# Performance work log

Measured on AMD Instinct MI355X. Metric: run time of the kernel, lower is better.

Reference implementation:

```python
import jax, jax.numpy as jnp
import numpy as np

N, E, G = 50000, 800000, 512
IN_DIM, EDGE_DIM, HID, OUT_DIM, HEADS = 16, 8, 32, 64, 4
NEG_SLOPE = 0.2


def _glorot(key, shape):
    fan_in, fan_out = shape[0], shape[-1]
    lim = jnp.sqrt(6.0 / (fan_in + fan_out))
    return jax.random.uniform(key, shape, jnp.float32, -lim, lim)


def setup_inputs() -> dict:
    key = jax.random.key(0)
    ks = jax.random.split(key, 32)
    inp = {
        "x": jax.random.normal(ks[0], (N, IN_DIM), jnp.float32),
        "edge_src": jax.random.randint(ks[1], (E,), 0, N, jnp.int32),
        "edge_dst": jax.random.randint(ks[2], (E,), 0, N, jnp.int32),
        "edge_attr": jax.random.normal(ks[3], (E, EDGE_DIM), jnp.float32),
        "batch": jnp.sort(jax.random.randint(ks[4], (N,), 0, G, jnp.int32)),
    }
    # layer 1: in=16 -> heads=4, C=32
    inp["W1s"] = _glorot(ks[5], (IN_DIM, HEADS * HID)); inp["W1d"] = _glorot(ks[6], (IN_DIM, HEADS * HID))
    inp["W1e"] = _glorot(ks[7], (EDGE_DIM, HEADS * HID))
    inp["b1s"] = jnp.zeros((HEADS * HID,)); inp["b1d"] = jnp.zeros((HEADS * HID,))
    inp["att1"] = _glorot(ks[8], (HEADS, HID)); inp["bias1"] = jnp.zeros((HEADS * HID,))
    # layer 2: in=128 -> heads=4, C=32
    D2 = HEADS * HID
    inp["W2s"] = _glorot(ks[9], (D2, HEADS * HID)); inp["W2d"] = _glorot(ks[10], (D2, HEADS * HID))
    inp["W2e"] = _glorot(ks[11], (EDGE_DIM, HEADS * HID))
    inp["b2s"] = jnp.zeros((HEADS * HID,)); inp["b2d"] = jnp.zeros((HEADS * HID,))
    inp["att2"] = _glorot(ks[12], (HEADS, HID)); inp["bias2"] = jnp.zeros((HEADS * HID,))
    # layer 3: in=128 -> heads=1, C=32
    inp["W3s"] = _glorot(ks[13], (D2, HID)); inp["W3d"] = _glorot(ks[14], (D2, HID))
    inp["W3e"] = _glorot(ks[15], (EDGE_DIM, HID))
    inp["b3s"] = jnp.zeros((HID,)); inp["b3d"] = jnp.zeros((HID,))
    inp["att3"] = _glorot(ks[16], (1, HID)); inp["bias3"] = jnp.zeros((HID,))
    # MLP: 32 -> 64 -> 64
    inp["Wm1"] = _glorot(ks[17], (HID, 2 * HID)); inp["bm1"] = jnp.zeros((2 * HID,))
    inp["Wm2"] = _glorot(ks[18], (2 * HID, OUT_DIM)); inp["bm2"] = jnp.zeros((OUT_DIM,))
    return inp


def gatv2_conv(x, src, dst, edge_attr, Ws, Wd, We, bs, bd, att, bias, heads, ch):
    n = x.shape[0]
    xs = (x @ Ws + bs).reshape(n, heads, ch)   # lin_l (source / value)
    xd = (x @ Wd + bd).reshape(n, heads, ch)   # lin_r (target)
    ea = (edge_attr @ We).reshape(-1, heads, ch)
    z = jax.nn.leaky_relu(xs[src] + xd[dst] + ea, NEG_SLOPE)       # [E,H,C]
    e = jnp.einsum('ehc,hc->eh', z, att)                           # [E,H]
    m = jax.ops.segment_max(e, dst, num_segments=n)                # scatter-softmax over dst
    p = jnp.exp(e - m[dst])
    denom = jax.ops.segment_sum(p, dst, num_segments=n)
    alpha = p / denom[dst]                                          # [E,H]
    msg = xs[src] * alpha[:, :, None]                               # [E,H,C]
    out = jax.ops.segment_sum(msg, dst, num_segments=n)
    return out.reshape(n, heads * ch) + bias


def reference(x, edge_src, edge_dst, edge_attr, batch,
              W1s, W1d, W1e, b1s, b1d, att1, bias1,
              W2s, W2d, W2e, b2s, b2d, att2, bias2,
              W3s, W3d, W3e, b3s, b3d, att3, bias3,
              Wm1, bm1, Wm2, bm2):
    h = jax.nn.elu(gatv2_conv(x, edge_src, edge_dst, edge_attr, W1s, W1d, W1e, b1s, b1d, att1, bias1, HEADS, HID))
    h = jax.nn.elu(gatv2_conv(h, edge_src, edge_dst, edge_attr, W2s, W2d, W2e, b2s, b2d, att2, bias2, HEADS, HID))
    h = gatv2_conv(h, edge_src, edge_dst, edge_attr, W3s, W3d, W3e, b3s, b3d, att3, bias3, 1, HID)
    # global mean pool over graphs
    sums = jax.ops.segment_sum(h, batch, num_segments=G)
    cnt = jax.ops.segment_sum(jnp.ones((h.shape[0],), h.dtype), batch, num_segments=G)
    emb = sums / jnp.maximum(cnt, 1.0)[:, None]
    return jax.nn.relu(emb @ Wm1 + bm1) @ Wm2 + bm2
```

## Files before the change

### kernel.cpp

```cpp
#include <hip/hip_runtime.h>
#include <cstdint>
#include <cstddef>

constexpr int kN = 50000;
constexpr int kE = 800000;
constexpr int kG = 512;
constexpr float kNegSlope = 0.2f;
constexpr float kLog2e = 1.4426950408889634f;

typedef float f4v __attribute__((ext_vector_type(4)));
typedef _Float16 h2v __attribute__((ext_vector_type(2)));
typedef _Float16 h4v __attribute__((ext_vector_type(4)));
typedef _Float16 h8v __attribute__((ext_vector_type(8)));

#if defined(__has_builtin)
#if __has_builtin(__builtin_amdgcn_fdot2)
#define HAS_FDOT2 1
#endif
#if __has_builtin(__builtin_amdgcn_exp2f)
#define HAS_EXP2 1
#endif
#endif

__device__ inline float dot2f(h2v a, h2v b, float c) {
#ifdef HAS_FDOT2
  return __builtin_amdgcn_fdot2(a, b, c, false);
#else
  return c + (float)a.x * (float)b.x + (float)a.y * (float)b.y;
#endif
}

#ifdef HAS_EXP2
#define ATT_SC kLog2e
__device__ inline float fexp(float x) { return __builtin_amdgcn_exp2f(x); }
#else
#define ATT_SC 1.0f
__device__ inline float fexp(float x) { return __expf(x); }
#endif


constexpr int kRec = 32;

__global__ void k_hist(const int* __restrict__ dst, int* __restrict__ counts,
                       int* __restrict__ pos, int n) {
  int i = blockIdx.x * blockDim.x + threadIdx.x;
  if (i < n) pos[i] = atomicAdd(&counts[dst[i]], 1);
}

__global__ __launch_bounds__(256) void k_scan_blk(const int* __restrict__ counts,
                                                  int* __restrict__ excl,
                                                  int* __restrict__ bsums, int n) {
  __shared__ int sh[256];
  int tid = threadIdx.x;
  int i = blockIdx.x * 256 + tid;
  int c = (i < n) ? counts[i] : 0;
  sh[tid] = c;
  __syncthreads();
  for (int off = 1; off < 256; off <<= 1) {
    int t = (tid >= off) ? sh[tid - off] : 0;
    __syncthreads();
    sh[tid] += t;
    __syncthreads();
  }
  if (i < n) excl[i] = sh[tid] - c;
  if (tid == 255) bsums[blockIdx.x] = sh[255];
}

__global__ __launch_bounds__(256) void k_scan_add(const int* __restrict__ excl,
                                                  const int* __restrict__ bsums,
                                                  int* __restrict__ row_ptr,
                                                  int n, int nb) {
  __shared__ int sh[256];
  int tid = threadIdx.x;
  int c = (tid < nb) ? bsums[tid] : 0;
  sh[tid] = c;
  __syncthreads();
  for (int off = 1; off < 256; off <<= 1) {
    int t = (tid >= off) ? sh[tid - off] : 0;
    __syncthreads();
    sh[tid] += t;
    __syncthreads();
  }
  int top = (blockIdx.x > 0) ? sh[blockIdx.x - 1] : 0;
  int total = sh[nb - 1];
  __syncthreads();
  int i = blockIdx.x * 256 + tid;
  if (i < n) row_ptr[i] = excl[i] + top;
  if (i == n) row_ptr[n] = total;
}

__global__ void k_scatter(const int* __restrict__ src, const int* __restrict__ dst,
                          const float* __restrict__ eattr,
                          const int* __restrict__ row_ptr, const int* __restrict__ pos,
                          char* __restrict__ csr, int n) {
  int i = blockIdx.x * blockDim.x + threadIdx.x;
  if (i >= n) return;
  int p = row_ptr[dst[i]] + pos[i];
  const float4* s4 = (const float4*)eattr + (size_t)i * 2;
  float4 a = s4[0];
  float4 b = s4[1];
  h8v hv;
  hv[0] = (_Float16)a.x; hv[1] = (_Float16)a.y; hv[2] = (_Float16)a.z; hv[3] = (_Float16)a.w;
  hv[4] = (_Float16)b.x; hv[5] = (_Float16)b.y; hv[6] = (_Float16)b.z; hv[7] = (_Float16)b.w;
  char* r = csr + (size_t)p * kRec;
  *(h8v*)r = hv;
  *(uint32_t*)(r + 16) = (uint32_t)src[i];
}

__global__ __launch_bounds__(256) void k_prep(
    const float* __restrict__ x,
    const float* __restrict__ W1s, const float* __restrict__ W1d,
    const float* __restrict__ W2s, const float* __restrict__ W2d,
    const float* __restrict__ W3s, const float* __restrict__ W3d,
    const float* __restrict__ W1e, const float* __restrict__ W2e,
    const float* __restrict__ W3e,
    const int* __restrict__ batch, int* __restrict__ gptr,
    int* __restrict__ counts,
    _Float16* __restrict__ xf, _Float16* __restrict__ Wt1,
    _Float16* __restrict__ Wt2, _Float16* __restrict__ Wt3,
    _Float16* __restrict__ We1t, _Float16* __restrict__ We2t,
    _Float16* __restrict__ We3t, int n) {
  int i = blockIdx.x * 256 + threadIdx.x;
  if (i < n) {
    counts[i] = 0;
    int b1 = batch[i];
    int b0 = (i == 0) ? -1 : batch[i - 1];
    for (int g = b0 + 1; g <= b1; ++g) gptr[g] = i;
    if (i == n - 1) {
      for (int g = b1 + 1; g <= kG; ++g) gptr[g] = n;
    }
  }
  i -= n;
  if (i < 0) return;
  int r0 = n * 4;
  if (i < r0) {
    int node = i >> 2, j = i & 3;
    h8v v;
    if (j < 2) {
      const float4* xp = (const float4*)(x + node * 16 + j * 8);
      float4 a = xp[0], b = xp[1];
      v[0] = (_Float16)a.x; v[1] = (_Float16)a.y; v[2] = (_Float16)a.z; v[3] = (_Float16)a.w;
      v[4] = (_Float16)b.x; v[5] = (_Float16)b.y; v[6] = (_Float16)b.z; v[7] = (_Float16)b.w;
    } else {
#pragma unroll
      for (int q = 0; q < 8; ++q) v[q] = (_Float16)0.f;
    }
    *(h8v*)(xf + (size_t)node * 32 + j * 8) = v;
    return;
  }
  i -= r0;
  if (i < 256 * 32) {
    int c = i >> 5, k = i & 31;
    const float* W = (c < 128) ? W1s : W1d;
    Wt1[i] = (k < 16) ? (_Float16)W[k * 128 + (c & 127)] : (_Float16)0.f;
    return;
  }
  i -= 256 * 32;
  if (i < 256 * 128) {
    int c = i >> 7, k = i & 127;
    const float* W = (c < 128) ? W2s : W2d;
    Wt2[i] = (_Float16)W[k * 128 + (c & 127)];
    return;
  }
  i -= 256 * 128;
  if (i < 64 * 128) {
    int c = i >> 7, k = i & 127;
    const float* W = (c < 32) ? W3s : W3d;
    int cc = (c < 32) ? c : c - 32;
    Wt3[i] = (_Float16)W[k * 32 + cc];
    return;
  }
  i -= 64 * 128;
  if (i < 128 * 8) {
    We1t[i] = (_Float16)W1e[(i & 7) * 128 + (i >> 3)];
    return;
  }
  i -= 128 * 8;
  if (i < 128 * 8) {
    We2t[i] = (_Float16)W2e[(i & 7) * 128 + (i >> 3)];
    return;
  }
  i -= 128 * 8;
  if (i < 32 * 8) {
    We3t[i] = (_Float16)W3e[(i & 7) * 32 + (i >> 3)];
  }
}

template <int KT, int NC2>
__global__ __launch_bounds__(256) void k_tmfma(
    const _Float16* __restrict__ hf, const _Float16* __restrict__ Wt,
    const float* __restrict__ bs, const float* __restrict__ bd,
    _Float16* __restrict__ xs_h, _Float16* __restrict__ xd_h, int n_nodes) {
  constexpr int K = KT * 32;
  constexpr int NCS = NC2 / 2;
  constexpr int D = NCS * 16;
  int lane = threadIdx.x & 63;
  int wid = threadIdx.x >> 6;
  int m = lane & 15;
  int quad = lane >> 4;
  int base = (blockIdx.x * 4 + wid) * 16;
  if (base >= n_nodes) return;
  int arow = min(base + m, n_nodes - 1);

  h8v a[KT];
#pragma unroll
  for (int t = 0; t < KT; ++t)
    a[t] = *(const h8v*)(hf + (size_t)arow * K + t * 32 + quad * 8);

  bool full = (base + 16 <= n_nodes);
#pragma unroll
  for (int c = 0; c < NC2; ++c) {
    f4v acc = {0.f, 0.f, 0.f, 0.f};
#pragma unroll
    for (int t = 0; t < KT; ++t) {
      h8v b = *(const h8v*)(Wt + (size_t)(c * 16 + m) * K + t * 32 + quad * 8);
      acc = __builtin_amdgcn_mfma_f32_16x16x32_f16(a[t], b, acc, 0, 0, 0);
    }
    float bv = (c < NCS) ? bs[c * 16 + m] : bd[(c - NCS) * 16 + m];
#pragma unroll
    for (int r = 0; r < 4; ++r) {
      int node = base + quad * 4 + r;
      if (full || node < n_nodes) {
        if (c < NCS)
          xs_h[(size_t)node * D + c * 16 + m] = (_Float16)(acc[r] + bv);
        else
          xd_h[(size_t)node * D + (c - NCS) * 16 + m] = (_Float16)(acc[r] + bv);
      }
    }
  }
}

template <bool DO_ELU>
__global__ __launch_bounds__(64) void k_gat128(
    const int* __restrict__ row_ptr, const char* __restrict__ csr,
    const _Float16* __restrict__ xs_h, const _Float16* __restrict__ xd_h,
    const float* __restrict__ att, const float* __restrict__ bias,
    const _Float16* __restrict__ Wet, _Float16* __restrict__ hout, int n_nodes) {
  __shared__ _Float16 sea[64 * 8];
  int lane = threadIdx.x & 63;
  int node = blockIdx.x;
  if (node >= n_nodes) return;
  int slot = lane >> 5;
  int sl = lane & 31;
  int ch0 = sl * 4;

  float4 at4 = *(const float4*)(att + ch0);
  float atl[4] = {at4.x * ATT_SC, at4.y * ATT_SC, at4.z * ATT_SC, at4.w * ATT_SC};
  h2v we[4][4];
#pragma unroll
  for (int c = 0; c < 4; ++c) {
    h8v wv = *(const h8v*)(Wet + (size_t)(ch0 + c) * 8);
#pragma unroll
    for (int t = 0; t < 4; ++t) {
      h2v w;
      w[0] = wv[2 * t];
      w[1] = wv[2 * t + 1];
      we[c][t] = w;
    }
  }
  float4 bv4 = *(const float4*)(bias + ch0);
  float bl[4] = {bv4.x, bv4.y, bv4.z, bv4.w};

  h4v xdh = *(const h4v*)(xd_h + (size_t)node * 128 + ch0);
  float xdl[4];
#pragma unroll
  for (int c = 0; c < 4; ++c) xdl[c] = (float)xdh[c];

  const char* xsb = (const char*)xs_h;
  uint32_t chb = (uint32_t)sl * 8u;

  float acc[4] = {0.f, 0.f, 0.f, 0.f};
  float l_run = 0.f;
  int beg = row_ptr[node], end = row_ptr[node + 1];

  for (int cbeg = beg; cbeg < end; cbeg += 64) {
    int cnt = min(end - cbeg, 64);
    int sv = 0;
    if (lane < cnt) {
      const char* r = csr + (size_t)(cbeg + lane) * kRec;
      h8v t = __builtin_nontemporal_load((const h8v*)r);
      sv = (int)__builtin_nontemporal_load((const uint32_t*)(r + 16));
      *(h8v*)&sea[lane * 8] = t;
    }

    auto addr = [&](int i) -> uint32_t {
      int s = __shfl(sv, i + slot, 64);
      return (uint32_t)s * 256u + chb;
    };
    auto consume = [&](int i, h4v xh) {
      int e = i + slot;
      const h2v* pe = (const h2v*)&sea[e * 8];
      h2v a0 = pe[0], a1 = pe[1], a2 = pe[2], a3 = pe[3];
      float xf[4];
#pragma unroll
      for (int c = 0; c < 4; ++c) xf[c] = (float)xh[c];
      float sc = 0.f;
#pragma unroll
      for (int c = 0; c < 4; ++c) {
        float z = dot2f(a3, we[c][3],
                  dot2f(a2, we[c][2],
                  dot2f(a1, we[c][1],
                  dot2f(a0, we[c][0], xf[c] + xdl[c]))));
        z = fmaxf(z, kNegSlope * z);
        sc = fmaf(z, atl[c], sc);
      }
      sc += __shfl_xor(sc, 1, 64);
      sc += __shfl_xor(sc, 2, 64);
      sc += __shfl_xor(sc, 4, 64);
      float p = (e < cnt) ? fexp(sc) : 0.f;
      l_run += p;
#pragma unroll
      for (int c = 0; c < 4; ++c) acc[c] += p * xf[c];
    };

    uint32_t oa = addr(0), ob = addr(2);
    h4v xa = *(const h4v*)(xsb + oa);
    h4v xb = *(const h4v*)(xsb + ob);
    for (int i = 0; i < cnt; i += 4) {
      bool pf = (i + 4 < cnt);
      h4v pa, pb;
      if (pf) {
        uint32_t na = addr(i + 4), nb = addr(i + 6);
        pa = *(const h4v*)(xsb + na);
        pb = *(const h4v*)(xsb + nb);
      }
      consume(i, xa);
      consume(i + 2, xb);
      if (pf) { xa = pa; xb = pb; }
    }
  }

  l_run += __shfl_xor(l_run, 32, 64);
#pragma unroll
  for (int c = 0; c < 4; ++c) acc[c] += __shfl_xor(acc[c], 32, 64);

  if (slot == 0) {
    float inv = (l_run > 0.f) ? (1.f / l_run) : 0.f;
    h4v ov;
#pragma unroll
    for (int c = 0; c < 4; ++c) {
      float o = acc[c] * inv + bl[c];
      if (DO_ELU) o = (o > 0.f) ? o : (__expf(o) - 1.f);
      ov[c] = (_Float16)o;
    }
    __builtin_nontemporal_store(ov, (h4v*)(hout + (size_t)node * 128 + ch0));
  }
}

template <bool DO_ELU>
__global__ __launch_bounds__(64) void k_gat32(
    const int* __restrict__ row_ptr, const char* __restrict__ csr,
    const _Float16* __restrict__ xs_h, const _Float16* __restrict__ xd_h,
    const float* __restrict__ att, const float* __restrict__ bias,
    const _Float16* __restrict__ Wet, _Float16* __restrict__ hout, int n_nodes) {
  __shared__ _Float16 sea[32 * 8];
  int lane = threadIdx.x & 63;
  int node = blockIdx.x;
  if (node >= n_nodes) return;
  int slot = lane >> 3;
  int sl = lane & 7;
  int ch0 = sl * 4;

  float4 at4 = *(const float4*)(att + ch0);
  float atl[4] = {at4.x * ATT_SC, at4.y * ATT_SC, at4.z * ATT_SC, at4.w * ATT_SC};
  h2v we[4][4];
#pragma unroll
  for (int c = 0; c < 4; ++c) {
    h8v wv = *(const h8v*)(Wet + (size_t)(ch0 + c) * 8);
#pragma unroll
    for (int t = 0; t < 4; ++t) {
      h2v w;
      w[0] = wv[2 * t];
      w[1] = wv[2 * t + 1];
      we[c][t] = w;
    }
  }
  float4 bv4 = *(const float4*)(bias + ch0);
  float bl[4] = {bv4.x, bv4.y, bv4.z, bv4.w};

  h4v xdh = *(const h4v*)(xd_h + (size_t)node * 32 + ch0);
  float xdl[4];
#pragma unroll
  for (int c = 0; c < 4; ++c) xdl[c] = (float)xdh[c];

  const char* xsb = (const char*)xs_h;
  uint32_t chb = (uint32_t)sl * 8u;

  float acc[4] = {0.f, 0.f, 0.f, 0.f};
  float l_run = 0.f;
  int beg = row_ptr[node], end = row_ptr[node + 1];

  for (int cbeg = beg; cbeg < end; cbeg += 32) {
    int cnt = min(end - cbeg, 32);
    int sv = 0;
    if (lane < cnt) {
      const char* r = csr + (size_t)(cbeg + lane) * kRec;
      h8v t = __builtin_nontemporal_load((const h8v*)r);
      sv = (int)__builtin_nontemporal_load((const uint32_t*)(r + 16));
      *(h8v*)&sea[lane * 8] = t;
    }

    auto addr = [&](int i) -> uint32_t {
      int idx = (i + slot) & 31;
      int s = __shfl(sv, idx, 64);
      return (uint32_t)s * 64u + chb;
    };
    auto consume = [&](int i, h4v xh) {
      int e = i + slot;
      const h2v* pe = (const h2v*)&sea[e * 8];
      h2v a0 = pe[0], a1 = pe[1], a2 = pe[2], a3 = pe[3];
      float xf[4];
#pragma unroll
      for (int c = 0; c < 4; ++c) xf[c] = (float)xh[c];
      float sc = 0.f;
#pragma unroll
      for (int c = 0; c < 4; ++c) {
        float z = dot2f(a3, we[c][3],
                  dot2f(a2, we[c][2],
                  dot2f(a1, we[c][1],
                  dot2f(a0, we[c][0], xf[c] + xdl[c]))));
        z = fmaxf(z, kNegSlope * z);
        sc = fmaf(z, atl[c], sc);
      }
      sc += __shfl_xor(sc, 1, 64);
      sc += __shfl_xor(sc, 2, 64);
      sc += __shfl_xor(sc, 4, 64);
      float p = (e < cnt) ? fexp(sc) : 0.f;
      l_run += p;
#pragma unroll
      for (int c = 0; c < 4; ++c) acc[c] += p * xf[c];
    };

    uint32_t oa = addr(0), ob = addr(8);
    h4v xa = *(const h4v*)(xsb + oa);
    h4v xb = *(const h4v*)(xsb + ob);
    for (int i = 0; i < cnt; i += 16) {
      bool pf = (i + 16 < cnt);
      h4v pa, pb;
      if (pf) {
        uint32_t na = addr(i + 16), nb = addr(i + 24);
        pa = *(const h4v*)(xsb + na);
        pb = *(const h4v*)(xsb + nb);
      }
      consume(i, xa);
      consume(i + 8, xb);
      if (pf) { xa = pa; xb = pb; }
    }
  }

#pragma unroll
  for (int off = 8; off < 64; off <<= 1) {
    l_run += __shfl_xor(l_run, off, 64);
#pragma unroll
    for (int c = 0; c < 4; ++c) acc[c] += __shfl_xor(acc[c], off, 64);
  }

  if (slot == 0) {
    float inv = (l_run > 0.f) ? (1.f / l_run) : 0.f;
    h4v ov;
#pragma unroll
    for (int c = 0; c < 4; ++c) {
      float o = acc[c] * inv + bl[c];
      if (DO_ELU) o = (o > 0.f) ? o : (__expf(o) - 1.f);
      ov[c] = (_Float16)o;
    }
    __builtin_nontemporal_store(ov, (h4v*)(hout + (size_t)node * 32 + ch0));
  }
}

__global__ __launch_bounds__(64) void k_pool_mlp(
    const _Float16* __restrict__ h3, const int* __restrict__ gptr,
    const float* __restrict__ Wm1, const float* __restrict__ bm1,
    const float* __restrict__ Wm2, const float* __restrict__ bm2,
    float* __restrict__ out, int n_nodes) {
  int g = blockIdx.x;
  int t = threadIdx.x;
  int lo = gptr[g];
  int hi = gptr[g + 1];
  int c = t & 31, half = t >> 5;
  float sum = 0.f;
  for (int i = lo + half; i < hi; i += 2) sum += (float)h3[(size_t)i * 32 + c];
  sum += __shfl_xor(sum, 32, 64);
  float cnt = (float)(hi - lo);
  float emb = sum / fmaxf(cnt, 1.f);
  __shared__ float sh_emb[32];
  __shared__ float sh_hid[64];
  if (half == 0) sh_emb[c] = emb;
  __syncthreads();
  float hv = bm1[t];
  for (int k = 0; k < 32; ++k) hv += sh_emb[k] * Wm1[k * 64 + t];
  hv = fmaxf(hv, 0.f);
  sh_hid[t] = hv;
  __syncthreads();
  float ov = bm2[t];
  for (int k = 0; k < 64; ++k) ov += sh_hid[k] * Wm2[k * 64 + t];
  out[(size_t)g * 64 + t] = ov;
}

extern "C" void kernel_launch(void* const* d_in, const int* in_sizes, int n_in,
                              void* d_out, int out_size, void* d_ws, size_t ws_size,
                              hipStream_t stream) {
  const float* x = (const float*)d_in[0];
  const int* esrc = (const int*)d_in[1];
  const int* edst = (const int*)d_in[2];
  const float* eattr = (const float*)d_in[3];
  const int* batch = (const int*)d_in[4];
  const float* W1s = (const float*)d_in[5];
  const float* W1d = (const float*)d_in[6];
  const float* W1e = (const float*)d_in[7];
  const float* b1s = (const float*)d_in[8];
  const float* b1d = (const float*)d_in[9];
  const float* att1 = (const float*)d_in[10];
  const float* bias1 = (const float*)d_in[11];
  const float* W2s = (const float*)d_in[12];
  const float* W2d = (const float*)d_in[13];
  const float* W2e = (const float*)d_in[14];
  const float* b2s = (const float*)d_in[15];
  const float* b2d = (const float*)d_in[16];
  const float* att2 = (const float*)d_in[17];
  const float* bias2 = (const float*)d_in[18];
  const float* W3s = (const float*)d_in[19];
  const float* W3d = (const float*)d_in[20];
  const float* W3e = (const float*)d_in[21];
  const float* b3s = (const float*)d_in[22];
  const float* b3d = (const float*)d_in[23];
  const float* att3 = (const float*)d_in[24];
  const float* bias3 = (const float*)d_in[25];
  const float* Wm1 = (const float*)d_in[26];
  const float* bm1 = (const float*)d_in[27];
  const float* Wm2 = (const float*)d_in[28];
  const float* bm2 = (const float*)d_in[29];

  constexpr int kNB = (kN + 255) / 256;

  char* p = (char*)d_ws;
  auto take = [&](size_t bytes) {
    char* r = p;
    p += (bytes + 255) & ~(size_t)255;
    return r;
  };
  int* row_ptr = (int*)take((size_t)(kN + 1) * sizeof(int));
  int* counts = (int*)take((size_t)kN * sizeof(int));
  int* pos = (int*)take((size_t)kE * sizeof(int));
  int* excl = (int*)take((size_t)kN * sizeof(int));
  int* bsums = (int*)take((size_t)kNB * sizeof(int));
  int* gptr = (int*)take((size_t)(kG + 1) * sizeof(int));
  char* csr = take((size_t)kE * kRec);
  _Float16* xf = (_Float16*)take((size_t)kN * 32 * sizeof(_Float16));
  _Float16* Wt1 = (_Float16*)take((size_t)256 * 32 * sizeof(_Float16));
  _Float16* Wt2 = (_Float16*)take((size_t)256 * 128 * sizeof(_Float16));
  _Float16* Wt3 = (_Float16*)take((size_t)64 * 128 * sizeof(_Float16));
  _Float16* We1t = (_Float16*)take((size_t)128 * 8 * sizeof(_Float16));
  _Float16* We2t = (_Float16*)take((size_t)128 * 8 * sizeof(_Float16));
  _Float16* We3t = (_Float16*)take((size_t)32 * 8 * sizeof(_Float16));
  _Float16* xs_h = (_Float16*)take((size_t)kN * 128 * sizeof(_Float16));
  _Float16* xd_h = (_Float16*)take((size_t)kN * 128 * sizeof(_Float16));
  _Float16* hA = (_Float16*)take((size_t)kN * 128 * sizeof(_Float16));
  _Float16* hB = (_Float16*)take((size_t)kN * 128 * sizeof(_Float16));
  _Float16* h3 = (_Float16*)take((size_t)kN * 32 * sizeof(_Float16));

  {
    int prep_total = kN + kN * 4 + 256 * 32 + 256 * 128 + 64 * 128 +
                     128 * 8 + 128 * 8 + 32 * 8;
    k_prep<<<(prep_total + 255) / 256, 256, 0, stream>>>(
        x, W1s, W1d, W2s, W2d, W3s, W3d, W1e, W2e, W3e,
        batch, gptr, counts, xf, Wt1, Wt2, Wt3, We1t, We2t, We3t, kN);
  }
  k_hist<<<(kE + 255) / 256, 256, 0, stream>>>(edst, counts, pos, kE);
  k_scan_blk<<<kNB, 256, 0, stream>>>(counts, excl, bsums, kN);
  k_scan_add<<<(kN + 1 + 255) / 256, 256, 0, stream>>>(excl, bsums, row_ptr, kN, kNB);
  k_scatter<<<(kE + 255) / 256, 256, 0, stream>>>(esrc, edst, eattr, row_ptr, pos,
                                                  csr, kE);

  constexpr int kTB = (kN + 63) / 64;

  k_tmfma<1, 16><<<kTB, 256, 0, stream>>>(xf, Wt1, b1s, b1d, xs_h, xd_h, kN);
  k_gat128<true><<<kN, 64, 0, stream>>>(row_ptr, csr, xs_h, xd_h,
                                        att1, bias1, We1t, hA, kN);
  k_tmfma<4, 16><<<kTB, 256, 0, stream>>>(hA, Wt2, b2s, b2d, xs_h, xd_h, kN);
  k_gat128<true><<<kN, 64, 0, stream>>>(row_ptr, csr, xs_h, xd_h,
                                        att2, bias2, We2t, hB, kN);
  k_tmfma<4, 4><<<kTB, 256, 0, stream>>>(hB, Wt3, b3s, b3d, xs_h, xd_h, kN);
  k_gat32<false><<<kN, 64, 0, stream>>>(row_ptr, csr, xs_h, xd_h,
                                        att3, bias3, We3t, h3, kN);
  k_pool_mlp<<<kG, 64, 0, stream>>>(h3, gptr, Wm1, bm1, Wm2, bm2, (float*)d_out, kN);
}
```

Before: 411.0 us.

## Drop nontemporal hints, write full CSR record tail, widen pooling kernel

Three unrelated tweaks. The CSR record tail is now written as one 16-byte store with zero padding instead of a lone 4-byte store, so each record fill is a full-line write. The GAT kernels switch their nontemporal loads and stores to ordinary ones, so CSR records and hidden activations that are reused across the three layers can stay in cache. The pool+MLP kernel grows from 64 to 256 threads, with 8 segments doing the per-graph sum and a shared-memory reduction, in exchange for extra barriers.

```diff
diff --git a/kernel.cpp b/kernel.cpp
--- a/kernel.cpp
+++ b/kernel.cpp
@@ -103,8 +103,10 @@
   hv[0] = (_Float16)a.x; hv[1] = (_Float16)a.y; hv[2] = (_Float16)a.z; hv[3] = (_Float16)a.w;
   hv[4] = (_Float16)b.x; hv[5] = (_Float16)b.y; hv[6] = (_Float16)b.z; hv[7] = (_Float16)b.w;
   char* r = csr + (size_t)p * kRec;
+  uint4 tail;
+  tail.x = (uint32_t)src[i]; tail.y = 0; tail.z = 0; tail.w = 0;
   *(h8v*)r = hv;
-  *(uint32_t*)(r + 16) = (uint32_t)src[i];
+  *(uint4*)(r + 16) = tail;
 }
 
 __global__ __launch_bounds__(256) void k_prep(
@@ -278,8 +280,8 @@
     int sv = 0;
     if (lane < cnt) {
       const char* r = csr + (size_t)(cbeg + lane) * kRec;
-      h8v t = __builtin_nontemporal_load((const h8v*)r);
-      sv = (int)__builtin_nontemporal_load((const uint32_t*)(r + 16));
+      h8v t = *(const h8v*)r;
+      sv = (int)*(const uint32_t*)(r + 16);
       *(h8v*)&sea[lane * 8] = t;
     }
 
@@ -343,7 +345,7 @@
       if (DO_ELU) o = (o > 0.f) ? o : (__expf(o) - 1.f);
       ov[c] = (_Float16)o;
     }
-    __builtin_nontemporal_store(ov, (h4v*)(hout + (size_t)node * 128 + ch0));
+    *(h4v*)(hout + (size_t)node * 128 + ch0) = ov;
   }
 }
 
@@ -395,8 +397,8 @@
     int sv = 0;
     if (lane < cnt) {
       const char* r = csr + (size_t)(cbeg + lane) * kRec;
-      h8v t = __builtin_nontemporal_load((const h8v*)r);
-      sv = (int)__builtin_nontemporal_load((const uint32_t*)(r + 16));
+      h8v t = *(const h8v*)r;
+      sv = (int)*(const uint32_t*)(r + 16);
       *(h8v*)&sea[lane * 8] = t;
     }
 
@@ -464,11 +466,11 @@
       if (DO_ELU) o = (o > 0.f) ? o : (__expf(o) - 1.f);
       ov[c] = (_Float16)o;
     }
-    __builtin_nontemporal_store(ov, (h4v*)(hout + (size_t)node * 32 + ch0));
-  }
-}
-
-__global__ __launch_bounds__(64) void k_pool_mlp(
+    *(h4v*)(hout + (size_t)node * 32 + ch0) = ov;
+  }
+}
+
+__global__ __launch_bounds__(256) void k_pool_mlp(
     const _Float16* __restrict__ h3, const int* __restrict__ gptr,
     const float* __restrict__ Wm1, const float* __restrict__ bm1,
     const float* __restrict__ Wm2, const float* __restrict__ bm2,
@@ -477,24 +479,33 @@
   int t = threadIdx.x;
   int lo = gptr[g];
   int hi = gptr[g + 1];
-  int c = t & 31, half = t >> 5;
+  int c = t & 31, seg = t >> 5;
   float sum = 0.f;
-  for (int i = lo + half; i < hi; i += 2) sum += (float)h3[(size_t)i * 32 + c];
-  sum += __shfl_xor(sum, 32, 64);
-  float cnt = (float)(hi - lo);
-  float emb = sum / fmaxf(cnt, 1.f);
+  for (int i = lo + seg; i < hi; i += 8) sum += (float)h3[(size_t)i * 32 + c];
+  __shared__ float psum[8][32];
   __shared__ float sh_emb[32];
   __shared__ float sh_hid[64];
-  if (half == 0) sh_emb[c] = emb;
+  psum[seg][c] = sum;
   __syncthreads();
-  float hv = bm1[t];
-  for (int k = 0; k < 32; ++k) hv += sh_emb[k] * Wm1[k * 64 + t];
-  hv = fmaxf(hv, 0.f);
-  sh_hid[t] = hv;
+  if (t < 32) {
+    float s = 0.f;
+#pragma unroll
+    for (int q = 0; q < 8; ++q) s += psum[q][t];
+    float cnt = (float)(hi - lo);
+    sh_emb[t] = s / fmaxf(cnt, 1.f);
+  }
   __syncthreads();
-  float ov = bm2[t];
-  for (int k = 0; k < 64; ++k) ov += sh_hid[k] * Wm2[k * 64 + t];
-  out[(size_t)g * 64 + t] = ov;
+  if (t < 64) {
+    float hv = bm1[t];
+    for (int k = 0; k < 32; ++k) hv += sh_emb[k] * Wm1[k * 64 + t];
+    sh_hid[t] = fmaxf(hv, 0.f);
+  }
+  __syncthreads();
+  if (t < 64) {
+    float ov = bm2[t];
+    for (int k = 0; k < 64; ++k) ov += sh_hid[k] * Wm2[k * 64 + t];
+    out[(size_t)g * 64 + t] = ov;
+  }
 }
 
 extern "C" void kernel_launch(void* const* d_in, const int* in_sizes, int n_in,
@@ -583,5 +594,5 @@
   k_tmfma<4, 4><<<kTB, 256, 0, stream>>>(hB, Wt3, b3s, b3d, xs_h, xd_h, kN);
   k_gat32<false><<<kN, 64, 0, stream>>>(row_ptr, csr, xs_h, xd_h,
                                         att3, bias3, We3t, h3, kN);
-  k_pool_mlp<<<kG, 64, 0, stream>>>(h3, gptr, Wm1, bm1, Wm2, bm2, (float*)d_out, kN);
-}
+  k_pool_mlp<<<kG, 256, 0, stream>>>(h3, gptr, Wm1, bm1, Wm2, bm2, (float*)d_out, kN);
+}
```

Measured after the change: 394.5 us. 1.04x faster.
